# Kernel optimization log

Hardware: AMD Instinct MI355X
Metric: run time of the kernel (lower is better)

Reference implementation:

```python
import jax, jax.numpy as jnp
import numpy as np

DIM = 512
HEADS = 8
DIM_HEAD = 64
INNER = HEADS * DIM_HEAD  # 512
NARROW_K = 9
WIDE_K = 9
WIDE_DIL = 5


def setup_inputs() -> dict:
    key = jax.random.key(0)
    ks = jax.random.split(key, 12)
    b, n = 4, 2048
    s = lambda fan_in: 1.0 / np.sqrt(fan_in)
    inp = {
        'tokens': jax.random.normal(ks[0], (b, n, DIM), jnp.float32),
        'mask': jax.random.randint(ks[1], (b, n), 0, 2) > 0,
        'w_qkv': jax.random.normal(ks[2], (DIM, INNER * 3), jnp.float32) * s(DIM),
        'w_out': jax.random.normal(ks[3], (INNER, DIM), jnp.float32) * s(INNER),
        'b_out': jnp.zeros((DIM,), jnp.float32),
        'w_narrow': jax.random.normal(ks[4], (DIM, DIM, NARROW_K), jnp.float32) * s(DIM * NARROW_K),
        'b_narrow': jnp.zeros((DIM,), jnp.float32),
        'w_wide': jax.random.normal(ks[5], (DIM, DIM, WIDE_K), jnp.float32) * s(DIM * WIDE_K),
        'b_wide': jnp.zeros((DIM,), jnp.float32),
        'ln1_g': jnp.ones((DIM,), jnp.float32),
        'ln1_b': jnp.zeros((DIM,), jnp.float32),
        'ff_w': jax.random.normal(ks[6], (DIM, DIM), jnp.float32) * s(DIM),
        'ff_b': jnp.zeros((DIM,), jnp.float32),
        'ln2_g': jnp.ones((DIM,), jnp.float32),
        'ln2_b': jnp.zeros((DIM,), jnp.float32),
    }
    return inp


def layer_norm(x, g, b, eps=1e-5):
    m = jnp.mean(x, axis=-1, keepdims=True)
    v = jnp.mean(jnp.square(x - m), axis=-1, keepdims=True)
    return (x - m) / jnp.sqrt(v + eps) * g + b


def rope_encoding(seq_len, dim_head, dtype):
    inv_freq = 1.0 / (10000.0 ** (jnp.arange(0, dim_head, 2, dtype=jnp.float32) / dim_head))
    pos = jnp.arange(seq_len, dtype=jnp.float32)
    sinu = jnp.einsum('i,j->ij', pos, inv_freq)  # [n, d/2]
    return jnp.concatenate([jnp.sin(sinu), jnp.cos(sinu)], axis=-1).astype(dtype)  # [n, d]


def attn(tokens, mask, w_qkv, w_out, b_out):
    b, n, _ = tokens.shape
    qkv = tokens @ w_qkv  # [b, n, 3*inner]
    q, k, v = jnp.split(qkv, 3, axis=-1)
    reshp = lambda t: t.reshape(b, n, HEADS, DIM_HEAD).transpose(0, 2, 1, 3)  # b h n d
    q, k, v = reshp(q), reshp(k), reshp(v)
    rope = rope_encoding(n, DIM_HEAD, tokens.dtype)  # [n, d]
    q = q + rope
    k = k + rope
    mask4 = mask[:, None, :, None]  # b 1 n 1
    big = jnp.finfo(k.dtype).max
    k = jnp.where(mask4, k, -big)
    q = jax.nn.softmax(q, axis=-1) * (DIM_HEAD ** -0.5)
    k = jax.nn.softmax(k, axis=2)  # over n
    v = jnp.where(mask4, v, 0.0)
    context = jnp.einsum('bhnd,bhne->bhde', k, v)
    out = jnp.einsum('bhde,bhnd->bhne', context, q)
    out = out.transpose(0, 2, 1, 3).reshape(b, n, INNER)
    return out @ w_out + b_out


def conv1d(x, w, b, padding, dilation):
    # x: [b, c, n], w: [out, in, k]
    y = jax.lax.conv_general_dilated(
        x, w, window_strides=(1,), padding=[(padding, padding)],
        rhs_dilation=(dilation,), dimension_numbers=('NCW', 'OIW', 'NCW'))
    return y + b[None, :, None]


def reference(tokens, mask, w_qkv, w_out, b_out, w_narrow, b_narrow,
              w_wide, b_wide, ln1_g, ln1_b, ff_w, ff_b, ln2_g, ln2_b):
    tokens = attn(tokens, mask, w_qkv, w_out, b_out)
    conv_in = tokens.transpose(0, 2, 1)  # b d n
    conv_in = jnp.where(mask[:, None, :], conv_in, 0.0)
    narrow = jax.nn.gelu(conv1d(conv_in, w_narrow, b_narrow, NARROW_K // 2, 1), approximate=False)
    wide_pad = (WIDE_K + (WIDE_K - 1) * (WIDE_DIL - 1)) // 2  # 20
    wide = jax.nn.gelu(conv1d(conv_in, w_wide, b_wide, wide_pad, WIDE_DIL), approximate=False)
    tokens = tokens + narrow.transpose(0, 2, 1) + wide.transpose(0, 2, 1)
    tokens = layer_norm(tokens, ln1_g, ln1_b)
    tokens = layer_norm(jax.nn.gelu(tokens @ ff_w + ff_b, approximate=False), ln2_g, ln2_b)
    return tokens
```

## Files before the change

### kernel.cpp

```cpp
#include <hip/hip_runtime.h>
#include <hip/hip_bf16.h>

#define BB 4
#define NN 2048
#define NROWS (BB*NN)

typedef unsigned short u16;
typedef __bf16 bf16x8 __attribute__((ext_vector_type(8)));
typedef u16    u16x8  __attribute__((ext_vector_type(8)));
typedef u16    u16x4  __attribute__((ext_vector_type(4)));
typedef float  fx4    __attribute__((ext_vector_type(4)));

__device__ __forceinline__ float bf2f(u16 u){
  union { float f; unsigned int i; } x; x.i = ((unsigned int)u) << 16; return x.f;
}
__device__ __forceinline__ u16 f2bf(float f){
  union { float f; unsigned int i; } x; x.f = f;
  unsigned int i = x.i;
  i += 0x7fffu + ((i >> 16) & 1u);
  return (u16)(i >> 16);
}
__device__ __forceinline__ float geluf(float x){
  return 0.5f * x * (1.0f + erff(x * 0.70710678118654752f));
}
__device__ __forceinline__ void gload16(const void* g, void* l){
  __builtin_amdgcn_global_load_lds((const __attribute__((address_space(1))) unsigned int*)g,
                                   (__attribute__((address_space(3))) unsigned int*)l, 16, 0, 0);
}

__global__ __launch_bounds__(256) void sniff_k(const u16* tokens, const unsigned int* mask, int* flags){
  __shared__ int s_f32, s_byte;
  if (threadIdx.x == 0) { s_f32 = 0; s_byte = 0; }
  __syncthreads();
  for (int i = threadIdx.x; i < 4096; i += 256) {
    float v = bf2f(tokens[i]);
    if (!(fabsf(v) < 1e10f)) atomicOr(&s_f32, 1);
  }
  for (int i = threadIdx.x; i < 2048; i += 256) {
    if (mask[i] > 1u) atomicOr(&s_byte, 1);
  }
  __syncthreads();
  if (threadIdx.x == 0) { flags[0] = s_f32; flags[1] = s_byte; }
}

__global__ __launch_bounds__(256) void misc2_k(const void* mask, const void* tokens,
                                               const void* p0, const void* p1, const void* p2,
                                               const void* p3, const void* p4, const void* p5,
                                               const void* p6, const void* p7,
                                               const int* flags, float* rope, int* m32,
                                               float* params, u16* tokbf,
                                               const void* w_qkv, const void* w_out, const void* ff_w,
                                               const void* w_narrow, const void* w_wide,
                                               u16* wqkvt, u16* woutt, u16* ffwt,
                                               u16* wtN2, u16* wtW2){
  int bid = blockIdx.x;
  int tid = threadIdx.x;
  int f = flags[0];
  if (bid < 2048) {
    const void* srcs[8] = {p0,p1,p2,p3,p4,p5,p6,p7};
    int mbyte = flags[1];
    const int T = 131072 + 8192 + 4096 + 1048576;
    for (int i = bid*256 + tid; i < T; i += 2048*256) {
      if (i < 131072) {
        int p = i >> 6, j = i & 63;
        int jj = (j < 32) ? j : j - 32;
        float invf = exp2f(-(float)jj * (13.287712379549449f/32.0f));
        float prod = (float)p * invf;
        rope[i] = (j < 32) ? sinf(prod) : cosf(prod);
      } else if (i < 139264) {
        int k = i - 131072;
        int v = mbyte ? (int)((const unsigned char*)mask)[k] : ((const int*)mask)[k];
        m32[k] = v ? 1 : 0;
      } else if (i < 143360) {
        int k = i - 139264;
        int pid = k >> 9, j = k & 511;
        const void* s = srcs[pid];
        params[k] = f ? ((const float*)s)[j] : bf2f(((const u16*)s)[j]);
      } else if (f) {
        int k4 = (i - 143360) * 4;
        float4 v = *(const float4*)&((const float*)tokens)[k4];
        u16x4 o;
        o[0] = f2bf(v.x); o[1] = f2bf(v.y); o[2] = f2bf(v.z); o[3] = f2bf(v.w);
        *(u16x4*)&tokbf[k4] = o;
      }
    }
  } else if (bid < 3072) {
    int id = bid - 2048;
    int tensor = id >> 9, o = id & 511;
    const void* src = tensor ? w_wide : w_narrow;
    u16* dst = tensor ? wtW2 : wtN2;
    __shared__ u16 Ls[4608];
    for (int i = tid; i < 4608; i += 256) {
      Ls[i] = f ? f2bf(((const float*)src)[(size_t)o*4608 + i]) : ((const u16*)src)[(size_t)o*4608 + i];
    }
    __syncthreads();
    #pragma unroll
    for (int kk = 0; kk < 9; kk++) {
      #pragma unroll
      for (int u = 0; u < 2; u++) {
        int c = tid + u*256;
        dst[(size_t)kk*262144 + o*512 + c] = Ls[c*9 + kk];
      }
    }
  } else {
    int id = bid - 3072;
    int z = id / 192;
    int rem = id - z*192;
    int x = rem % 24, y = rem / 24;
    int Nn = (z == 0) ? 1536 : 512;
    if (x * 64 >= Nn) return;
    const void* src = (z == 0) ? w_qkv : (z == 1) ? w_out : ff_w;
    u16* dst = (z == 0) ? wqkvt : (z == 1) ? woutt : ffwt;
    __shared__ u16 Ts[64][72];
    int n0 = x * 64, k0 = y * 64;
    int r = tid >> 2, cq = (tid & 3) * 16;
    #pragma unroll
    for (int u = 0; u < 2; u++) {
      int c = cq + u*8;
      int sidx = (k0 + r)*Nn + n0 + c;
      u16x8 v;
      if (f) {
        #pragma unroll
        for (int j = 0; j < 8; j++) v[j] = f2bf(((const float*)src)[sidx + j]);
      } else {
        v = *(const u16x8*)&((const u16*)src)[sidx];
      }
      *(u16x8*)&Ts[r][c] = v;
    }
    __syncthreads();
    #pragma unroll
    for (int u = 0; u < 2; u++) {
      int c = cq + u*8;
      u16x8 v;
      #pragma unroll
      for (int j = 0; j < 8; j++) v[j] = Ts[c + j][r];
      *(u16x8*)&dst[(size_t)(n0 + r)*512 + k0 + c] = v;
    }
  }
}

__global__ __launch_bounds__(256) void mgemm_qkv_k(const void* tok_raw, const u16* tokbf,
                                                   const u16* Bt, const float* rope,
                                                   const int* mask, const int* flags,
                                                   u16* qb, u16* keb, u16* vb){
  __shared__ u16 As[128*32];
  __shared__ u16 Bs[128*32];
  __shared__ int smask[128];
  int tid = threadIdx.x;
  int lane = tid & 63;
  int wave = tid >> 6;
  int wm = (wave >> 1) * 64, wn = (wave & 1) * 64;
  int quad = lane >> 4, l16 = lane & 15;
  int m0 = blockIdx.y * 128, n0 = blockIdx.x * 128;
  const u16* A = flags[0] ? tokbf : (const u16*)tok_raw;
  fx4 acc[4][4] = {};
  for (int k0 = 0; k0 < 512; k0 += 32) {
    #pragma unroll
    for (int it = 0; it < 2; it++) {
      int s = it*256 + tid;
      int lsl = ((s & 3) ^ ((s >> 3) & 3)) * 8;
      gload16(&A[(size_t)(m0 + (s >> 2))*512 + k0 + lsl], &As[(it*256 + wave*64)*8]);
    }
    #pragma unroll
    for (int it = 0; it < 2; it++) {
      int s = it*256 + tid;
      int lsl = ((s & 3) ^ ((s >> 3) & 3)) * 8;
      gload16(&Bt[(size_t)(n0 + (s >> 2))*512 + k0 + lsl], &Bs[(it*256 + wave*64)*8]);
    }
    __syncthreads();
    bf16x8 af[4], bfv[4];
    #pragma unroll
    for (int i = 0; i < 4; i++) {
      int row = wm + i*16 + l16;
      af[i] = __builtin_bit_cast(bf16x8,
                *(const u16x8*)&As[row*32 + ((quad ^ ((row >> 1) & 3)) * 8)]);
    }
    #pragma unroll
    for (int j = 0; j < 4; j++) {
      int row = wn + j*16 + l16;
      bfv[j] = __builtin_bit_cast(bf16x8,
                *(const u16x8*)&Bs[row*32 + ((quad ^ ((row >> 1) & 3)) * 8)]);
    }
    #pragma unroll
    for (int i = 0; i < 4; i++)
      #pragma unroll
      for (int j = 0; j < 4; j++)
        acc[i][j] = __builtin_amdgcn_mfma_f32_16x16x32_bf16(af[i], bfv[j], acc[i][j], 0, 0, 0);
    __syncthreads();
  }
  int x = blockIdx.x;
  if (x >= 4) {
    if (tid < 128) smask[tid] = mask[m0 + tid];
    __syncthreads();
  }
  if (x < 4) {
    #pragma unroll
    for (int i = 0; i < 4; i++)
      #pragma unroll
      for (int r = 0; r < 4; r++) {
        int rl = wm + i*16 + quad*4 + r;
        int row = m0 + rl;
        int nseq = row & (NN-1);
        const float* rp = rope + nseq*64 + l16;
        float e0 = __expf(acc[i][0][r] + rp[0]);
        float e1 = __expf(acc[i][1][r] + rp[16]);
        float e2 = __expf(acc[i][2][r] + rp[32]);
        float e3 = __expf(acc[i][3][r] + rp[48]);
        float s = e0 + e1 + e2 + e3;
        s += __shfl_xor(s, 1); s += __shfl_xor(s, 2);
        s += __shfl_xor(s, 4); s += __shfl_xor(s, 8);
        float sc = 0.125f / s;
        size_t base = (size_t)row*512 + n0 + wn + l16;
        qb[base]      = f2bf(e0*sc);
        qb[base + 16] = f2bf(e1*sc);
        qb[base + 32] = f2bf(e2*sc);
        qb[base + 48] = f2bf(e3*sc);
      }
  } else if (x < 8) {
    #pragma unroll
    for (int i = 0; i < 4; i++)
      #pragma unroll
      for (int r = 0; r < 4; r++) {
        int rl = wm + i*16 + quad*4 + r;
        int row = m0 + rl;
        int nseq = row & (NN-1);
        int mk = smask[rl];
        const float* rp = rope + nseq*64 + l16;
        size_t base = (size_t)row*512 + (n0 - 512) + wn + l16;
        #pragma unroll
        for (int j = 0; j < 4; j++) {
          float ke = mk ? __expf(acc[i][j][r] + rp[j*16]) : 0.0f;
          keb[base + j*16] = f2bf(ke);
        }
      }
  } else {
    #pragma unroll
    for (int i = 0; i < 4; i++)
      #pragma unroll
      for (int r = 0; r < 4; r++) {
        int rl = wm + i*16 + quad*4 + r;
        int row = m0 + rl;
        int mk = smask[rl];
        size_t base = (size_t)row*512 + (n0 - 1024) + wn + l16;
        #pragma unroll
        for (int j = 0; j < 4; j++)
          vb[base + j*16] = mk ? f2bf(acc[i][j][r]) : (u16)0;
      }
  }
}

#define FMA16(a, b, acc) \
  acc[0][0] = fmaf(a.x, b.x, acc[0][0]); acc[0][1] = fmaf(a.x, b.y, acc[0][1]); \
  acc[0][2] = fmaf(a.x, b.z, acc[0][2]); acc[0][3] = fmaf(a.x, b.w, acc[0][3]); \
  acc[1][0] = fmaf(a.y, b.x, acc[1][0]); acc[1][1] = fmaf(a.y, b.y, acc[1][1]); \
  acc[1][2] = fmaf(a.y, b.z, acc[1][2]); acc[1][3] = fmaf(a.y, b.w, acc[1][3]); \
  acc[2][0] = fmaf(a.z, b.x, acc[2][0]); acc[2][1] = fmaf(a.z, b.y, acc[2][1]); \
  acc[2][2] = fmaf(a.z, b.z, acc[2][2]); acc[2][3] = fmaf(a.z, b.w, acc[2][3]); \
  acc[3][0] = fmaf(a.w, b.x, acc[3][0]); acc[3][1] = fmaf(a.w, b.y, acc[3][1]); \
  acc[3][2] = fmaf(a.w, b.z, acc[3][2]); acc[3][3] = fmaf(a.w, b.w, acc[3][3]);

__global__ __launch_bounds__(256) void ctx_k(const u16* keb, const u16* vb, float* ctxp, float* Sgp){
  int bh = blockIdx.x, seg = blockIdx.y;
  int b = bh >> 3, h = bh & 7;
  __shared__ float Ks[32][68], Vs[32][68];
  __shared__ float sS[64];
  int tid = threadIdx.x, tx = tid & 15, ty = tid >> 4;
  if (tid < 64) sS[tid] = 0.0f;
  float acc[4][4] = {{0.f,0.f,0.f,0.f},{0.f,0.f,0.f,0.f},{0.f,0.f,0.f,0.f},{0.f,0.f,0.f,0.f}};
  float sp[8] = {0,0,0,0,0,0,0,0};
  int nl = tid >> 3, dcol = (tid & 7)*8;
  const u16* kp0 = keb + (size_t)(b*NN + seg*128)*512 + h*64 + dcol;
  const u16* vp0 = vb  + (size_t)(b*NN + seg*128)*512 + h*64 + dcol;
  for (int nc = 0; nc < 128; nc += 32) {
    u16x8 ku = *(const u16x8*)(kp0 + (size_t)(nc + nl)*512);
    u16x8 vu = *(const u16x8*)(vp0 + (size_t)(nc + nl)*512);
    float a[8], bb[8];
    #pragma unroll
    for (int t = 0; t < 8; t++) { a[t] = bf2f(ku[t]); bb[t] = bf2f(vu[t]); sp[t] += a[t]; }
    *(float4*)&Ks[nl][dcol]   = (float4){a[0],a[1],a[2],a[3]};
    *(float4*)&Ks[nl][dcol+4] = (float4){a[4],a[5],a[6],a[7]};
    *(float4*)&Vs[nl][dcol]   = (float4){bb[0],bb[1],bb[2],bb[3]};
    *(float4*)&Vs[nl][dcol+4] = (float4){bb[4],bb[5],bb[6],bb[7]};
    __syncthreads();
    #pragma unroll
    for (int q = 0; q < 32; q++) {
      float4 a4 = *(const float4*)&Ks[q][ty*4];
      float4 b4 = *(const float4*)&Vs[q][tx*4];
      FMA16(a4, b4, acc)
    }
    __syncthreads();
  }
  #pragma unroll
  for (int j = 0; j < 8; j++) atomicAdd(&sS[dcol + j], sp[j]);
  float* cp = ctxp + ((size_t)seg*32 + bh)*4096;
  #pragma unroll
  for (int i = 0; i < 4; i++)
    #pragma unroll
    for (int j = 0; j < 4; j++)
      cp[(ty*4 + i)*64 + tx*4 + j] = acc[i][j];
  __syncthreads();
  if (tid < 64) Sgp[(size_t)seg*2048 + bh*64 + tid] = sS[tid];
}

__global__ __launch_bounds__(256) void ctxw_k(const float* ctxp, const float* Sgp, const u16* woutt,
                                              u16* W2t, u16* cpadb){
  int bx = blockIdx.x;
  int tid = threadIdx.x;
  if (bx >= 32) {
    int idx = (bx - 32)*256 + tid;
    if (idx < BB*40*512) {
      int c = idx & 511;
      int t = (idx >> 9) % 40;
      int b = idx / (40*512);
      int tt = (t < 20) ? t : 2048 + t;
      cpadb[((size_t)b*2088 + tt)*512 + c] = 0;
    }
    return;
  }
  int h = bx & 7, b = bx >> 3;
  int lane = tid & 63, wave = tid >> 6;
  int quad = lane >> 4, l16 = lane & 15;
  int bh = b*8 + h;
  float rs[4];
  #pragma unroll
  for (int j = 0; j < 4; j++) {
    int d = j*16 + l16;
    float S = 0.0f;
    #pragma unroll
    for (int s = 0; s < 16; s++) S += Sgp[(size_t)s*2048 + bh*64 + d];
    rs[j] = (S > 0.0f) ? 1.0f/S : 0.0f;
  }
  fx4 acc[8][4] = {};
  #pragma unroll
  for (int ks = 0; ks < 2; ks++) {
    bf16x8 bfv[4];
    #pragma unroll
    for (int j = 0; j < 4; j++) {
      int d = j*16 + l16;
      fx4 v0 = {}, v1 = {};
      #pragma unroll
      for (int s = 0; s < 16; s++) {
        const float* src = ctxp + ((size_t)s*32 + bh)*4096 + d*64 + ks*32 + quad*8;
        v0 += *(const fx4*)src;
        v1 += *(const fx4*)(src + 4);
      }
      float r = rs[j];
      bf16x8 t;
      t[0]=(__bf16)(v0[0]*r); t[1]=(__bf16)(v0[1]*r); t[2]=(__bf16)(v0[2]*r); t[3]=(__bf16)(v0[3]*r);
      t[4]=(__bf16)(v1[0]*r); t[5]=(__bf16)(v1[1]*r); t[6]=(__bf16)(v1[2]*r); t[7]=(__bf16)(v1[3]*r);
      bfv[j] = t;
    }
    #pragma unroll
    for (int i = 0; i < 8; i++) {
      int orow = wave*128 + i*16 + l16;
      bf16x8 afr = __builtin_bit_cast(bf16x8, *(const u16x8*)&woutt[(size_t)orow*512 + h*64 + ks*32 + quad*8]);
      #pragma unroll
      for (int j = 0; j < 4; j++)
        acc[i][j] = __builtin_amdgcn_mfma_f32_16x16x32_bf16(afr, bfv[j], acc[i][j], 0, 0, 0);
    }
  }
  u16* out = W2t + (size_t)b*262144;
  #pragma unroll
  for (int i = 0; i < 8; i++)
    #pragma unroll
    for (int j = 0; j < 4; j++)
      #pragma unroll
      for (int r = 0; r < 4; r++) {
        int orow = wave*128 + i*16 + quad*4 + r;
        out[(size_t)orow*512 + h*64 + j*16 + l16] = f2bf(acc[i][j][r]);
      }
}

__global__ __launch_bounds__(256) void mgemm_attn64_k(const u16* qb, const u16* W2t, const float* bias,
                                                      const int* mask, u16* attnb, u16* cpadb){
  __shared__ u16 As[64][40];
  __shared__ u16 Bs[128][40];
  int tid = threadIdx.x;
  int lane = tid & 63;
  int wave = tid >> 6;
  int wn = wave * 32;
  int quad = lane >> 4, l16 = lane & 15;
  int m0 = blockIdx.y * 64, n0 = blockIdx.x * 128, b = blockIdx.z;
  const u16* A  = qb  + (size_t)b*2048*512;
  const u16* Bt = W2t + (size_t)b*262144;
  fx4 acc[4][2] = {};
  int ar = tid >> 2;
  int ac = (tid & 3) * 8;
  for (int k0 = 0; k0 < 512; k0 += 32) {
    *(u16x8*)&As[ar][ac]    = *(const u16x8*)&A[(size_t)(m0+ar)*512 + k0 + ac];
    *(u16x8*)&Bs[ar][ac]    = *(const u16x8*)&Bt[(size_t)(n0+ar)*512 + k0 + ac];
    *(u16x8*)&Bs[ar+64][ac] = *(const u16x8*)&Bt[(size_t)(n0+ar+64)*512 + k0 + ac];
    __syncthreads();
    bf16x8 af[4], bfv[2];
    #pragma unroll
    for (int i = 0; i < 4; i++)
      af[i] = __builtin_bit_cast(bf16x8, *(const u16x8*)&As[i*16 + l16][quad*8]);
    #pragma unroll
    for (int j = 0; j < 2; j++)
      bfv[j] = __builtin_bit_cast(bf16x8, *(const u16x8*)&Bs[wn + j*16 + l16][quad*8]);
    #pragma unroll
    for (int i = 0; i < 4; i++)
      #pragma unroll
      for (int j = 0; j < 2; j++)
        acc[i][j] = __builtin_amdgcn_mfma_f32_16x16x32_bf16(af[i], bfv[j], acc[i][j], 0, 0, 0);
    __syncthreads();
  }
  #pragma unroll
  for (int i = 0; i < 4; i++)
    #pragma unroll
    for (int j = 0; j < 2; j++) {
      int col = n0 + wn + j*16 + l16;
      float bv = bias[col];
      #pragma unroll
      for (int r = 0; r < 4; r++) {
        int row_l = m0 + i*16 + quad*4 + r;
        float v = acc[i][j][r] + bv;
        u16 vbb = f2bf(v);
        attnb[((size_t)b*2048 + row_l)*512 + col] = vbb;
        int mk = mask[b*2048 + row_l];
        cpadb[((size_t)b*2088 + row_l + 20)*512 + col] = mk ? vbb : (u16)0;
      }
    }
}

#define A_ROWS 552
#define A_SZ (A_ROWS*32)
#define W_SZ (9*64*32)
__global__ __launch_bounds__(512, 2) void mconv15_k(const u16* cpad, const u16* Wn, const u16* Ww,
                                                    const float* bias_n, const float* bias_w,
                                                    u16* Dn, u16* Dw){
  __shared__ u16 As[2*A_SZ];
  __shared__ u16 Ws[2*W_SZ];
  int tid = threadIdx.x;
  int lane = tid & 63;
  int wave = tid >> 6;
  int wm = wave * 64;
  int quad = lane >> 4, l16 = lane & 15;
  int o0 = blockIdx.x * 64, m0 = blockIdx.y * 512;
  int b = blockIdx.z >> 1, cid = blockIdx.z & 1;
  const u16* W = cid ? Ww : Wn;
  const float* bias = cid ? bias_w : bias_n;
  u16* D = cid ? Dw : Dn;
  fx4 acc[4][4] = {};
  const u16* cb = cpad + ((size_t)b*2088 + m0)*512;
  int wslot = ((quad ^ ((l16 >> 1) & 3)) * 8);
  int sbase = cid ? 0 : 16;
  int sstep = cid ? 5 : 1;
  int rowb0 = sbase + wm + l16;

  const u16* ap[5]; bool av[5];
  #pragma unroll
  for (int it = 0; it < 5; it++) {
    int s = it*512 + tid;
    av[it] = (s < 2208);
    int row = av[it] ? (s >> 2) : 0;
    int lsl = ((s & 3) ^ ((s >> 3) & 3)) * 8;
    ap[it] = cb + (size_t)row*512 + lsl;
  }
  const u16* wp[5]; bool wv[5];
  #pragma unroll
  for (int it = 0; it < 5; it++) {
    int s = it*512 + tid;
    wv[it] = (s < 2304);
    int kk = wv[it] ? (s >> 8) : 0;
    int ow = (s >> 2) & 63;
    int lsl = ((s & 3) ^ ((s >> 3) & 3)) * 8;
    wp[it] = W + (size_t)kk*262144 + (size_t)(o0 + ow)*512 + lsl;
  }

#define STAGE_CHUNK(c0, buf)                                                          \
  {                                                                                   \
    _Pragma("unroll")                                                                 \
    for (int it = 0; it < 5; it++) {                                                  \
      if (av[it])                                                                     \
        gload16(ap[it] + (c0), &As[(buf)*A_SZ + (it*512 + wave*64)*8]);               \
    }                                                                                 \
    _Pragma("unroll")                                                                 \
    for (int it = 0; it < 5; it++) {                                                  \
      if (wv[it])                                                                     \
        gload16(wp[it] + (c0), &Ws[(buf)*W_SZ + (it*512 + wave*64)*8]);               \
    }                                                                                 \
  }

#define LOADFRAG(kk, bfv, afr)                                                        \
  {                                                                                   \
    int rowb = rowb0 + sstep*(kk);                                                    \
    int aslot = ((quad ^ ((rowb >> 1) & 3)) * 8);                                     \
    _Pragma("unroll")                                                                 \
    for (int j = 0; j < 4; j++)                                                       \
      bfv[j] = __builtin_bit_cast(bf16x8,                                             \
                 *(const u16x8*)&Wsb[((kk)*64 + j*16 + l16)*32 + wslot]);             \
    _Pragma("unroll")                                                                 \
    for (int i = 0; i < 4; i++)                                                       \
      afr[i] = __builtin_bit_cast(bf16x8,                                             \
                 *(const u16x8*)&Asb[(rowb + i*16)*32 + aslot]);                      \
  }

#define MFMATAP_SGB(bfv, afr)                                                         \
  {                                                                                   \
    _Pragma("unroll")                                                                 \
    for (int i = 0; i < 4; i++)                                                       \
      _Pragma("unroll")                                                               \
      for (int j = 0; j < 4; j++)                                                     \
        acc[i][j] = __builtin_amdgcn_mfma_f32_16x16x32_bf16(afr[i], bfv[j],           \
                                                            acc[i][j], 0, 0, 0);      \
    _Pragma("unroll")                                                                 \
    for (int g = 0; g < 8; g++) {                                                     \
      __builtin_amdgcn_sched_group_barrier(0x008, 2, 0);                  \
      __builtin_amdgcn_sched_group_barrier(0x100, 1, 0);               \
    }                                                                                 \
  }

#define MFMATAP_PLAIN(bfv, afr)                                                       \
  {                                                                                   \
    _Pragma("unroll")                                                                 \
    for (int i = 0; i < 4; i++)                                                       \
      _Pragma("unroll")                                                               \
      for (int j = 0; j < 4; j++)                                                     \
        acc[i][j] = __builtin_amdgcn_mfma_f32_16x16x32_bf16(afr[i], bfv[j],           \
                                                            acc[i][j], 0, 0, 0);      \
  }

  STAGE_CHUNK(0, 0)
  __syncthreads();

  for (int ch = 0; ch < 16; ch++) {
    int cur = ch & 1;
    const u16* Asb = &As[cur*A_SZ];
    const u16* Wsb = &Ws[cur*W_SZ];
    bf16x8 bfvA[4], afrA[4], bfvB[4], afrB[4];
    LOADFRAG(0, bfvA, afrA)
    if (ch < 15) {
      int c0n = (ch + 1) * 32;
      int nb = cur ^ 1;
      STAGE_CHUNK(c0n, nb)
    }
    #pragma unroll
    for (int kt = 0; kt < 8; kt += 2) {
      LOADFRAG(kt+1, bfvB, afrB)
      MFMATAP_SGB(bfvA, afrA)
      LOADFRAG(kt+2, bfvA, afrA)
      MFMATAP_SGB(bfvB, afrB)
    }
    MFMATAP_PLAIN(bfvA, afrA)
    __syncthreads();
  }
#undef STAGE_CHUNK
#undef LOADFRAG
#undef MFMATAP_SGB
#undef MFMATAP_PLAIN
  #pragma unroll
  for (int i = 0; i < 4; i++)
    #pragma unroll
    for (int j = 0; j < 4; j++) {
      int col = o0 + j*16 + l16;
      float bv = bias[col];
      #pragma unroll
      for (int r = 0; r < 4; r++) {
        int row = b*2048 + m0 + wm + i*16 + quad*4 + r;
        D[(size_t)row*512 + col] = f2bf(geluf(acc[i][j][r] + bv));
      }
    }
}

__global__ __launch_bounds__(512) void mgemm128b_k(const u16* A, const u16* Bt, const float* bias,
                                                   u16* C){
  __shared__ u16 As[128*32];
  __shared__ u16 Bs[128*32];
  int tid = threadIdx.x;
  int lane = tid & 63;
  int wave = tid >> 6;
  int wm = (wave >> 2) * 64;
  int wn = (wave & 3) * 32;
  int quad = lane >> 4, l16 = lane & 15;
  int m0 = blockIdx.y * 128, n0 = blockIdx.x * 128;
  fx4 acc[4][2] = {};
  for (int k0 = 0; k0 < 512; k0 += 32) {
    {
      int s = tid;
      int lsl = ((s & 3) ^ ((s >> 3) & 3)) * 8;
      gload16(&A[(size_t)(m0 + (s >> 2))*512 + k0 + lsl], &As[(wave*64)*8]);
    }
    {
      int s = tid;
      int lsl = ((s & 3) ^ ((s >> 3) & 3)) * 8;
      gload16(&Bt[(size_t)(n0 + (s >> 2))*512 + k0 + lsl], &Bs[(wave*64)*8]);
    }
    __syncthreads();
    bf16x8 af[4], bfv[2];
    #pragma unroll
    for (int i = 0; i < 4; i++) {
      int row = wm + i*16 + l16;
      af[i] = __builtin_bit_cast(bf16x8,
                *(const u16x8*)&As[row*32 + ((quad ^ ((row >> 1) & 3)) * 8)]);
    }
    #pragma unroll
    for (int j = 0; j < 2; j++) {
      int row = wn + j*16 + l16;
      bfv[j] = __builtin_bit_cast(bf16x8,
                *(const u16x8*)&Bs[row*32 + ((quad ^ ((row >> 1) & 3)) * 8)]);
    }
    #pragma unroll
    for (int i = 0; i < 4; i++)
      #pragma unroll
      for (int j = 0; j < 2; j++)
        acc[i][j] = __builtin_amdgcn_mfma_f32_16x16x32_bf16(af[i], bfv[j], acc[i][j], 0, 0, 0);
    __syncthreads();
  }
  #pragma unroll
  for (int i = 0; i < 4; i++)
    #pragma unroll
    for (int j = 0; j < 2; j++) {
      int col = n0 + wn + j*16 + l16;
      float bv = bias[col];
      #pragma unroll
      for (int r = 0; r < 4; r++) {
        int row = m0 + wm + i*16 + quad*4 + r;
        C[(size_t)row*512 + col] = f2bf(geluf(acc[i][j][r] + bv));
      }
    }
}

template<int NADD, int OM>
__global__ __launch_bounds__(256) void lnw_k(const u16* X, const u16* Y, const u16* Z,
                                             const float* g, const float* be,
                                             const int* flags, void* out){
  int wave = threadIdx.x >> 6, lane = threadIdx.x & 63;
  size_t row = (size_t)blockIdx.x*4 + wave;
  int c = lane*8;
  float x[8];
  {
    u16x8 xv = *(const u16x8*)&X[row*512 + c];
    #pragma unroll
    for (int t = 0; t < 8; t++) x[t] = bf2f(xv[t]);
  }
  if (NADD >= 1) {
    u16x8 yv = *(const u16x8*)&Y[row*512 + c];
    #pragma unroll
    for (int t = 0; t < 8; t++) x[t] += bf2f(yv[t]);
  }
  if (NADD >= 2) {
    u16x8 zv = *(const u16x8*)&Z[row*512 + c];
    #pragma unroll
    for (int t = 0; t < 8; t++) x[t] += bf2f(zv[t]);
  }
  float s = 0.0f;
  #pragma unroll
  for (int t = 0; t < 8; t++) s += x[t];
  #pragma unroll
  for (int o = 32; o; o >>= 1) s += __shfl_xor(s, o, 64);
  float mean = s * (1.0f/512.0f);
  float d[8], s2 = 0.0f;
  #pragma unroll
  for (int t = 0; t < 8; t++) { d[t] = x[t] - mean; s2 += d[t]*d[t]; }
  #pragma unroll
  for (int o = 32; o; o >>= 1) s2 += __shfl_xor(s2, o, 64);
  float inv = rsqrtf(s2 * (1.0f/512.0f) + 1e-5f);
  float4 g0 = *(const float4*)&g[c],  g1 = *(const float4*)&g[c+4];
  float4 b0 = *(const float4*)&be[c], b1 = *(const float4*)&be[c+4];
  float r[8];
  r[0] = d[0]*inv*g0.x + b0.x; r[1] = d[1]*inv*g0.y + b0.y;
  r[2] = d[2]*inv*g0.z + b0.z; r[3] = d[3]*inv*g0.w + b0.w;
  r[4] = d[4]*inv*g1.x + b1.x; r[5] = d[5]*inv*g1.y + b1.y;
  r[6] = d[6]*inv*g1.z + b1.z; r[7] = d[7]*inv*g1.w + b1.w;
  bool obf = (OM == 1) || (OM == 2 && !flags[0]);
  if (obf) {
    u16x8 ov;
    #pragma unroll
    for (int t = 0; t < 8; t++) ov[t] = f2bf(r[t]);
    *(u16x8*)&((u16*)out)[row*512 + c] = ov;
  } else {
    float* op = (float*)out + row*512 + c;
    *(float4*)op       = (float4){r[0], r[1], r[2], r[3]};
    *(float4*)(op + 4) = (float4){r[4], r[5], r[6], r[7]};
  }
}

extern "C" void kernel_launch(void* const* d_in, const int* in_sizes, int n_in,
                              void* d_out, int out_size, void* d_ws, size_t ws_size,
                              hipStream_t stream) {
  const void* tokens   = d_in[0];
  const void* mask     = d_in[1];
  const void* w_qkv    = d_in[2];
  const void* w_out    = d_in[3];
  const void* b_out    = d_in[4];
  const void* w_narrow = d_in[5];
  const void* b_narrow = d_in[6];
  const void* w_wide   = d_in[7];
  const void* b_wide   = d_in[8];
  const void* ln1_g    = d_in[9];
  const void* ln1_b    = d_in[10];
  const void* ff_w     = d_in[11];
  const void* ff_b     = d_in[12];
  const void* ln2_g    = d_in[13];
  const void* ln2_b    = d_in[14];

  float* ws = (float*)d_ws;
  int*   flags  = (int*)ws;
  int*   m32    = (int*)(ws + 16);
  float* params = ws + 8208;
  float* kS     = ws + 12304;
  float* ctx    = ws + 14352;
  float* rope   = ws + 145424;
  u16*   tokbf  = (u16*)(ws + 276496);
  u16*   wqkvt  = (u16*)(ws + 2373648);
  u16*   woutt  = (u16*)(ws + 2766864);
  u16*   ffwt   = (u16*)(ws + 2897936);
  u16*   wtN2   = (u16*)(ws + 3029008);
  u16*   wtW2   = (u16*)(ws + 4208656);
  u16*   qb     = (u16*)(ws + 5388304);
  u16*   keb    = (u16*)(ws + 7485456);
  u16*   vb     = (u16*)(ws + 9582608);
  u16*   W2t    = (u16*)(ws + 11679760);
  u16*   attnb  = (u16*)(ws + 12204048);
  u16*   cpadb  = (u16*)(ws + 14301200);
  u16*   Dnb    = (u16*)(ws + 16439312);
  u16*   Dwb    = (u16*)(ws + 18536464);
  u16*   Eb     = attnb;
  u16*   t1b    = tokbf;
  float* ctxp   = (float*)Dnb;
  float* Sgp    = (float*)Dwb;

  float* p_bout = params;        float* p_bnar = params + 512;
  float* p_bwid = params + 1024; float* p_l1g  = params + 1536;
  float* p_l1b  = params + 2048; float* p_ffb  = params + 2560;
  float* p_l2g  = params + 3072; float* p_l2b  = params + 3584;

  sniff_k<<<dim3(1), dim3(256), 0, stream>>>((const u16*)tokens, (const unsigned int*)mask, flags);

  misc2_k<<<dim3(3648), dim3(256), 0, stream>>>(mask, tokens, b_out, b_narrow, b_wide, ln1_g, ln1_b,
                                                ff_b, ln2_g, ln2_b, flags, rope, m32, params,
                                                tokbf, w_qkv, w_out, ff_w, w_narrow, w_wide,
                                                wqkvt, woutt, ffwt, wtN2, wtW2);

  mgemm_qkv_k<<<dim3(12, 64), dim3(256), 0, stream>>>(
      tokens, tokbf, wqkvt, rope, m32, flags, qb, keb, vb);

  ctx_k<<<dim3(32, 16), dim3(256), 0, stream>>>(keb, vb, ctxp, Sgp);

  ctxw_k<<<dim3(352), dim3(256), 0, stream>>>(ctxp, Sgp, woutt, W2t, cpadb);

  mgemm_attn64_k<<<dim3(4, 32, 4), dim3(256), 0, stream>>>(qb, W2t, p_bout, m32, attnb, cpadb);

  mconv15_k<<<dim3(8, 4, 8), dim3(512), 0, stream>>>(cpadb, wtN2, wtW2, p_bnar, p_bwid, Dnb, Dwb);

  lnw_k<2,1><<<dim3(NROWS/4), dim3(256), 0, stream>>>(attnb, Dnb, Dwb, p_l1g, p_l1b, flags, (void*)t1b);

  mgemm128b_k<<<dim3(4, 64), dim3(512), 0, stream>>>(t1b, ffwt, p_ffb, Eb);

  lnw_k<0,2><<<dim3(NROWS/4), dim3(256), 0, stream>>>(Eb, nullptr, nullptr, p_l2g, p_l2b, flags, d_out);
}
```

Measured before the change: 337.7 us.

## Accumulate attention context via atomics instead of per-segment partials

The K^T V context kernel now covers 256-row segments with 8 blocks per head instead of 16, and adds its partial results straight into a single zeroed context buffer and key-sum buffer with atomicAdd. The misc kernel gains extra blocks that zero these buffers. The goal is to drop the 16-way partial reduction reads in ctxw_k and the large partial-buffer writes. In exchange it takes on global atomic contention, fewer blocks in ctx_k, and a float summation order that is no longer deterministic.

```diff
diff --git a/kernel.cpp b/kernel.cpp
--- a/kernel.cpp
+++ b/kernel.cpp
@@ -48,7 +48,7 @@
                                                const void* p3, const void* p4, const void* p5,
                                                const void* p6, const void* p7,
                                                const int* flags, float* rope, int* m32,
-                                               float* params, u16* tokbf,
+                                               float* params, float* ctx, float* kS, u16* tokbf,
                                                const void* w_qkv, const void* w_out, const void* ff_w,
                                                const void* w_narrow, const void* w_wide,
                                                u16* wqkvt, u16* woutt, u16* ffwt,
@@ -56,11 +56,11 @@
   int bid = blockIdx.x;
   int tid = threadIdx.x;
   int f = flags[0];
-  if (bid < 2048) {
+  if (bid < 4096) {
     const void* srcs[8] = {p0,p1,p2,p3,p4,p5,p6,p7};
     int mbyte = flags[1];
-    const int T = 131072 + 8192 + 4096 + 1048576;
-    for (int i = bid*256 + tid; i < T; i += 2048*256) {
+    const int T = 276480 + 1048576;
+    for (int i = bid*256 + tid; i < T; i += 4096*256) {
       if (i < 131072) {
         int p = i >> 6, j = i & 63;
         int jj = (j < 32) ? j : j - 32;
@@ -76,16 +76,20 @@
         int pid = k >> 9, j = k & 511;
         const void* s = srcs[pid];
         params[k] = f ? ((const float*)s)[j] : bf2f(((const u16*)s)[j]);
+      } else if (i < 274432) {
+        ctx[i - 143360] = 0.0f;
+      } else if (i < 276480) {
+        kS[i - 274432] = 0.0f;
       } else if (f) {
-        int k4 = (i - 143360) * 4;
+        int k4 = (i - 276480) * 4;
         float4 v = *(const float4*)&((const float*)tokens)[k4];
         u16x4 o;
         o[0] = f2bf(v.x); o[1] = f2bf(v.y); o[2] = f2bf(v.z); o[3] = f2bf(v.w);
         *(u16x4*)&tokbf[k4] = o;
       }
     }
-  } else if (bid < 3072) {
-    int id = bid - 2048;
+  } else if (bid < 5120) {
+    int id = bid - 4096;
     int tensor = id >> 9, o = id & 511;
     const void* src = tensor ? w_wide : w_narrow;
     u16* dst = tensor ? wtW2 : wtN2;
@@ -103,7 +107,7 @@
       }
     }
   } else {
-    int id = bid - 3072;
+    int id = bid - 5120;
     int z = id / 192;
     int rem = id - z*192;
     int x = rem % 24, y = rem / 24;
@@ -259,7 +263,7 @@
   acc[3][0] = fmaf(a.w, b.x, acc[3][0]); acc[3][1] = fmaf(a.w, b.y, acc[3][1]); \
   acc[3][2] = fmaf(a.w, b.z, acc[3][2]); acc[3][3] = fmaf(a.w, b.w, acc[3][3]);
 
-__global__ __launch_bounds__(256) void ctx_k(const u16* keb, const u16* vb, float* ctxp, float* Sgp){
+__global__ __launch_bounds__(256) void ctx_k(const u16* keb, const u16* vb, float* ctx, float* Sg){
   int bh = blockIdx.x, seg = blockIdx.y;
   int b = bh >> 3, h = bh & 7;
   __shared__ float Ks[32][68], Vs[32][68];
@@ -269,9 +273,9 @@
   float acc[4][4] = {{0.f,0.f,0.f,0.f},{0.f,0.f,0.f,0.f},{0.f,0.f,0.f,0.f},{0.f,0.f,0.f,0.f}};
   float sp[8] = {0,0,0,0,0,0,0,0};
   int nl = tid >> 3, dcol = (tid & 7)*8;
-  const u16* kp0 = keb + (size_t)(b*NN + seg*128)*512 + h*64 + dcol;
-  const u16* vp0 = vb  + (size_t)(b*NN + seg*128)*512 + h*64 + dcol;
-  for (int nc = 0; nc < 128; nc += 32) {
+  const u16* kp0 = keb + (size_t)(b*NN + seg*256)*512 + h*64 + dcol;
+  const u16* vp0 = vb  + (size_t)(b*NN + seg*256)*512 + h*64 + dcol;
+  for (int nc = 0; nc < 256; nc += 32) {
     u16x8 ku = *(const u16x8*)(kp0 + (size_t)(nc + nl)*512);
     u16x8 vu = *(const u16x8*)(vp0 + (size_t)(nc + nl)*512);
     float a[8], bb[8];
@@ -292,17 +296,17 @@
   }
   #pragma unroll
   for (int j = 0; j < 8; j++) atomicAdd(&sS[dcol + j], sp[j]);
-  float* cp = ctxp + ((size_t)seg*32 + bh)*4096;
+  float* cp = ctx + (size_t)bh*4096;
   #pragma unroll
   for (int i = 0; i < 4; i++)
     #pragma unroll
     for (int j = 0; j < 4; j++)
-      cp[(ty*4 + i)*64 + tx*4 + j] = acc[i][j];
+      atomicAdd(&cp[(ty*4 + i)*64 + tx*4 + j], acc[i][j]);
   __syncthreads();
-  if (tid < 64) Sgp[(size_t)seg*2048 + bh*64 + tid] = sS[tid];
-}
-
-__global__ __launch_bounds__(256) void ctxw_k(const float* ctxp, const float* Sgp, const u16* woutt,
+  if (tid < 64) atomicAdd(&Sg[bh*64 + tid], sS[tid]);
+}
+
+__global__ __launch_bounds__(256) void ctxw_k(const float* ctx, const float* Sg, const u16* woutt,
                                               u16* W2t, u16* cpadb){
   int bx = blockIdx.x;
   int tid = threadIdx.x;
@@ -320,16 +324,7 @@
   int h = bx & 7, b = bx >> 3;
   int lane = tid & 63, wave = tid >> 6;
   int quad = lane >> 4, l16 = lane & 15;
-  int bh = b*8 + h;
-  float rs[4];
-  #pragma unroll
-  for (int j = 0; j < 4; j++) {
-    int d = j*16 + l16;
-    float S = 0.0f;
-    #pragma unroll
-    for (int s = 0; s < 16; s++) S += Sgp[(size_t)s*2048 + bh*64 + d];
-    rs[j] = (S > 0.0f) ? 1.0f/S : 0.0f;
-  }
+  const float* cp = ctx + (size_t)(b*8 + h)*4096;
   fx4 acc[8][4] = {};
   #pragma unroll
   for (int ks = 0; ks < 2; ks++) {
@@ -337,17 +332,13 @@
     #pragma unroll
     for (int j = 0; j < 4; j++) {
       int d = j*16 + l16;
-      fx4 v0 = {}, v1 = {};
-      #pragma unroll
-      for (int s = 0; s < 16; s++) {
-        const float* src = ctxp + ((size_t)s*32 + bh)*4096 + d*64 + ks*32 + quad*8;
-        v0 += *(const fx4*)src;
-        v1 += *(const fx4*)(src + 4);
-      }
-      float r = rs[j];
+      float S = Sg[(b*8 + h)*64 + d];
+      float rs = (S > 0.0f) ? 1.0f/S : 0.0f;
+      const float* src = cp + d*64 + ks*32 + quad*8;
+      float4 v0 = *(const float4*)src, v1 = *(const float4*)(src + 4);
       bf16x8 t;
-      t[0]=(__bf16)(v0[0]*r); t[1]=(__bf16)(v0[1]*r); t[2]=(__bf16)(v0[2]*r); t[3]=(__bf16)(v0[3]*r);
-      t[4]=(__bf16)(v1[0]*r); t[5]=(__bf16)(v1[1]*r); t[6]=(__bf16)(v1[2]*r); t[7]=(__bf16)(v1[3]*r);
+      t[0]=(__bf16)(v0.x*rs); t[1]=(__bf16)(v0.y*rs); t[2]=(__bf16)(v0.z*rs); t[3]=(__bf16)(v0.w*rs);
+      t[4]=(__bf16)(v1.x*rs); t[5]=(__bf16)(v1.y*rs); t[6]=(__bf16)(v1.z*rs); t[7]=(__bf16)(v1.w*rs);
       bfv[j] = t;
     }
     #pragma unroll
@@ -718,8 +709,6 @@
   u16*   Dwb    = (u16*)(ws + 18536464);
   u16*   Eb     = attnb;
   u16*   t1b    = tokbf;
-  float* ctxp   = (float*)Dnb;
-  float* Sgp    = (float*)Dwb;
 
   float* p_bout = params;        float* p_bnar = params + 512;
   float* p_bwid = params + 1024; float* p_l1g  = params + 1536;
@@ -728,17 +717,17 @@
 
   sniff_k<<<dim3(1), dim3(256), 0, stream>>>((const u16*)tokens, (const unsigned int*)mask, flags);
 
-  misc2_k<<<dim3(3648), dim3(256), 0, stream>>>(mask, tokens, b_out, b_narrow, b_wide, ln1_g, ln1_b,
-                                                ff_b, ln2_g, ln2_b, flags, rope, m32, params,
-                                                tokbf, w_qkv, w_out, ff_w, w_narrow, w_wide,
+  misc2_k<<<dim3(5696), dim3(256), 0, stream>>>(mask, tokens, b_out, b_narrow, b_wide, ln1_g, ln1_b,
+                                                ff_b, ln2_g, ln2_b, flags, rope, m32, params, ctx,
+                                                kS, tokbf, w_qkv, w_out, ff_w, w_narrow, w_wide,
                                                 wqkvt, woutt, ffwt, wtN2, wtW2);
 
   mgemm_qkv_k<<<dim3(12, 64), dim3(256), 0, stream>>>(
       tokens, tokbf, wqkvt, rope, m32, flags, qb, keb, vb);
 
-  ctx_k<<<dim3(32, 16), dim3(256), 0, stream>>>(keb, vb, ctxp, Sgp);
-
-  ctxw_k<<<dim3(352), dim3(256), 0, stream>>>(ctxp, Sgp, woutt, W2t, cpadb);
+  ctx_k<<<dim3(32, 8), dim3(256), 0, stream>>>(keb, vb, ctx, kS);
+
+  ctxw_k<<<dim3(352), dim3(256), 0, stream>>>(ctx, kS, woutt, W2t, cpadb);
 
   mgemm_attn64_k<<<dim3(4, 32, 4), dim3(256), 0, stream>>>(qb, W2t, p_bout, m32, attnb, cpadb);
 
```

Result: faster. 317.0 us (median of 3 runs) (-6.1%).
